# Performance work log

Measured on AMD Instinct MI355X. Metric: run time of the kernel, lower is better.

The kernel has to match this reference:

```python
import jax, jax.numpy as jnp
import numpy as np

P = 16  # patch_size


def _tokenize(x, p):
    # (B,C,H,W) -> (B,C,nP,p,p), row-major patch order
    B, C, H, W = x.shape
    nH, nW = H // p, W // p
    x = x.reshape(B, C, nH, p, nW, p).transpose(0, 1, 2, 4, 3, 5)
    return x.reshape(B, C, nH * nW, p, p)


def _untokenize(t, p, H, W):
    B, C, nP, _, _ = t.shape
    nH, nW = H // p, W // p
    t = t.reshape(B, C, nH, nW, p, p).transpose(0, 1, 2, 4, 3, 5)
    return t.reshape(B, C, H, W)


def _sinusoidal_pe(n, d):
    pos = jnp.arange(n, dtype=jnp.float32)[:, None]                    # (n,1)
    div = jnp.exp(jnp.arange(0, d, 2, dtype=jnp.float32) * (-jnp.log(10000.0) / d))
    ang = pos * div                                                     # (n, d/2)
    pe = jnp.zeros((n, d), dtype=jnp.float32)
    pe = pe.at[:, 0::2].set(jnp.sin(ang))
    pe = pe.at[:, 1::2].set(jnp.cos(ang)[:, : d // 2])
    return pe


def setup_inputs() -> dict:
    key = jax.random.key(0)
    ks = jax.random.split(key, 7)
    B, C, H, W = 16, 3, 512, 512
    nh = 12
    D = C * P * P            # 768 token dim
    dh = D // nh             # 64 head dim
    s = 0.02
    x = jax.random.normal(ks[0], (B, C, H, W), dtype=jnp.float32)
    Wq = jax.random.normal(ks[1], (nh, D, dh), dtype=jnp.float32) * s
    Wk = jax.random.normal(ks[2], (nh, D, dh), dtype=jnp.float32) * s
    Wv = jax.random.normal(ks[3], (nh, D, dh), dtype=jnp.float32) * s
    bq = jax.random.normal(ks[4], (nh, dh), dtype=jnp.float32) * s
    bk = jax.random.normal(ks[5], (nh, dh), dtype=jnp.float32) * s
    bv = jax.random.normal(ks[6], (nh, dh), dtype=jnp.float32) * s
    return {"x": x, "Wq": Wq, "bq": bq, "Wk": Wk, "bk": bk, "Wv": Wv, "bv": bv}


def reference(x, Wq, bq, Wk, bk, Wv, bv):
    B, C, H, W = x.shape
    nh, D, dh = Wq.shape
    tok = _tokenize(x, P)                      # (B,C,nP,p,p)
    nP = tok.shape[2]
    t = tok.reshape(B, nP, D)                  # torch .view semantics (row-major reshape)
    pe = _sinusoidal_pe(nP, D)
    t = 2.0 * t + pe[None]
    # batched per-head projections (H heads, independent weights)
    q = jnp.einsum('bnd,hde->bhne', t, Wq) + bq[None, :, None, :]
    k = jnp.einsum('bnd,hde->bhne', t, Wk) + bk[None, :, None, :]
    v = jnp.einsum('bnd,hde->bhne', t, Wv) + bv[None, :, None, :]
    scores = jnp.einsum('bhne,bhme->bhnm', q, k) / jnp.sqrt(jnp.float32(dh))
    attn = jax.nn.softmax(scores, axis=-1)
    o = jnp.einsum('bhnm,bhme->bhne', attn, v)  # (B,nh,nP,dh)
    # concat heads along last dim
    out = o.transpose(0, 2, 1, 3).reshape(B, nP, D)
    out = out.reshape(B, C, nP, P, P)          # torch .view back
    return _untokenize(out, P, H, W)
```

## Files before the change

kernel.cpp:

```cpp
#include <hip/hip_runtime.h>
#include <hip/hip_bf16.h>
#include <math.h>

typedef short bf16x8 __attribute__((ext_vector_type(8)));
typedef float f32x4 __attribute__((ext_vector_type(4)));

static __device__ __forceinline__ unsigned short f2bf(float f) {
  unsigned int u = __float_as_uint(f);
  u += 0x7FFFu + ((u >> 16) & 1u);
  return (unsigned short)(u >> 16);
}

__global__ __launch_bounds__(256) void k_prep_w(const float* __restrict__ Wq,
                                                const float* __restrict__ Wk,
                                                const float* __restrict__ Wv,
                                                unsigned short* __restrict__ wt) {
  __shared__ unsigned short lw[64][72];
  int sh = blockIdx.x;
  int kt = blockIdx.y;
  int s = sh / 12, h = sh - s * 12;
  const float* W = (s == 0 ? Wq : (s == 1 ? Wk : Wv)) + h * 49152 + (kt << 6) * 64;
  int tid = threadIdx.x;
#pragma unroll
  for (int it = 0; it < 4; ++it) {
    int idx = it * 256 + tid;
    int kk = idx >> 4, e4 = (idx & 15) << 2;
    float4 v = *(const float4*)(W + kk * 64 + e4);
    lw[e4 + 0][kk] = f2bf(v.x);
    lw[e4 + 1][kk] = f2bf(v.y);
    lw[e4 + 2][kk] = f2bf(v.z);
    lw[e4 + 3][kk] = f2bf(v.w);
  }
  __syncthreads();
  unsigned short* outp = wt + sh * 49152 + (kt << 6);
#pragma unroll
  for (int it = 0; it < 2; ++it) {
    int c = it * 256 + tid;
    int e = c >> 3, kc = (c & 7) << 3;
    *(uint4*)(outp + e * 768 + kc) = *(const uint4*)&lw[e][kc];
  }
}

__global__ __launch_bounds__(256) void k_build_t(const float* __restrict__ x,
                                                 unsigned short* __restrict__ t) {
  int g = blockIdx.x * 256 + threadIdx.x;
  int f = g << 3;
  int m  = f / 768;
  int d  = f - m * 768;
  int c  = f >> 18;
  int rl = f & 262143;
  int n  = rl >> 8;
  int qq = rl & 255;
  int ii = qq >> 4, jj = qq & 15;
  float pe8[8];
#pragma unroll
  for (int u = 0; u < 8; ++u) {
    int dd = d + u;
    int k = dd >> 1;
    float ang = (float)m * expf(-0.023985261385f * (float)k);
    pe8[u] = (dd & 1) ? cosf(ang) : sinf(ang);
  }
  const float* xp0 = x + (c << 18) + (((n >> 5) << 4) + ii) * 512 + ((n & 31) << 4) + jj;
  for (int b = 0; b < 16; ++b) {
    const float* xp = xp0 + b * 786432;
    float4 v0 = *(const float4*)xp;
    float4 v1 = *(const float4*)(xp + 4);
    float xv[8] = {v0.x, v0.y, v0.z, v0.w, v1.x, v1.y, v1.z, v1.w};
    unsigned short tmp[8];
#pragma unroll
    for (int u = 0; u < 8; ++u) tmp[u] = f2bf(2.0f * xv[u] + pe8[u]);
    *(uint4*)(t + b * 786432 + f) = *(const uint4*)tmp;
  }
}

union SMQKV {
  struct { unsigned short tA[128][40]; unsigned short tB[64][40]; } g;
  unsigned short tr[64][136];
};
__global__ __launch_bounds__(256) void k_qkv(
    const unsigned short* __restrict__ t, const unsigned short* __restrict__ wt,
    const float* __restrict__ bq, const float* __restrict__ bk, const float* __restrict__ bv,
    unsigned short* __restrict__ qout, unsigned short* __restrict__ kout,
    unsigned short* __restrict__ vout) {
  __shared__ SMQKV sm;
  int bid = blockIdx.x;
  int xcd = bid & 7, idx = bid >> 3;
  int rt = xcd * 16 + idx / 36;
  int hs = idx % 36;
  int h = hs / 3, s = hs - h * 3;
  const unsigned short* Wp = wt + (s * 12 + h) * 49152;
  const float* bias = (s == 0 ? bq : (s == 1 ? bk : bv)) + h * 64;
  unsigned short* outp = (s == 0 ? qout : (s == 1 ? kout : vout));
  int tid = threadIdx.x, lane = tid & 63, w = tid >> 6;
  int row0 = rt << 7;
  f32x4 acc[2][4] = {};
  for (int k0 = 0; k0 < 768; k0 += 32) {
    __syncthreads();
#pragma unroll
    for (int it = 0; it < 2; ++it) {
      int idx2 = it * 256 + tid;
      int rr = idx2 >> 2, kq = (idx2 & 3) << 3;
      *(uint4*)&sm.g.tA[rr][kq] = *(const uint4*)(t + (row0 + rr) * 768 + k0 + kq);
    }
    {
      int e = tid >> 2, kc = (tid & 3) << 3;
      *(uint4*)&sm.g.tB[e][kc] = *(const uint4*)(Wp + e * 768 + k0 + kc);
    }
    __syncthreads();
    bf16x8 a0 = *(const bf16x8*)&sm.g.tA[w * 32 + (lane & 15)][(lane >> 4) << 3];
    bf16x8 a1 = *(const bf16x8*)&sm.g.tA[w * 32 + 16 + (lane & 15)][(lane >> 4) << 3];
#pragma unroll
    for (int cb = 0; cb < 4; ++cb) {
      bf16x8 bb = *(const bf16x8*)&sm.g.tB[cb * 16 + (lane & 15)][(lane >> 4) << 3];
      acc[0][cb] = __builtin_amdgcn_mfma_f32_16x16x32_bf16(a0, bb, acc[0][cb], 0, 0, 0);
      acc[1][cb] = __builtin_amdgcn_mfma_f32_16x16x32_bf16(a1, bb, acc[1][cb], 0, 0, 0);
    }
  }
  int bb2 = row0 >> 10;
  int n0 = row0 & 1023;
  int base = (bb2 * 12 + h) << 16;
  if (s < 2) {
    float qs = (s == 0) ? 0.18033688011f : 1.0f;
#pragma unroll
    for (int mt = 0; mt < 2; ++mt)
#pragma unroll
      for (int cb = 0; cb < 4; ++cb) {
        int e = cb * 16 + (lane & 15);
        float be = bias[e];
#pragma unroll
        for (int r = 0; r < 4; ++r) {
          int n = n0 + w * 32 + mt * 16 + ((lane >> 4) << 2) + r;
          outp[base + (n << 6) + e] = f2bf((acc[mt][cb][r] + be) * qs);
        }
      }
  } else {
    __syncthreads();
#pragma unroll
    for (int mt = 0; mt < 2; ++mt)
#pragma unroll
      for (int cb = 0; cb < 4; ++cb) {
        int e = cb * 16 + (lane & 15);
        float be = bias[e];
#pragma unroll
        for (int r = 0; r < 4; ++r) {
          int rr = w * 32 + ((lane >> 4) << 3) + mt * 4 + r;
          sm.tr[e][rr] = f2bf(acc[mt][cb][r] + be);
        }
      }
    __syncthreads();
#pragma unroll
    for (int it = 0; it < 4; ++it) {
      int c = it * 256 + tid;
      int e = c >> 4, nc = (c & 15) << 3;
      *(uint4*)(vout + base + (e << 10) + n0 + nc) = *(const uint4*)&sm.tr[e][nc];
    }
  }
}

__global__ __launch_bounds__(256) void k_attn(
    const unsigned short* __restrict__ Q,
    const unsigned short* __restrict__ K,
    const unsigned short* __restrict__ Vg,
    float* __restrict__ out) {
  __shared__ unsigned short Kt[64][72];
  __shared__ unsigned short Vt[80][72];
  int bid = blockIdx.x;
  int xcd = bid & 7, idx = bid >> 3;
  int bh = xcd * 24 + (idx >> 3);
  int qt = idx & 7;
  int b = bh / 12, h = bh - b * 12;
  int tid = threadIdx.x, lane = tid & 63, w = tid >> 6;
  int g = lane >> 4, q16 = lane & 15;
  int base = bh << 16;
  const unsigned short* Qp = Q + base + (qt << 7) * 64;
  const unsigned short* Kp = K + base;
  const unsigned short* Vp = Vg + base;
  {
    int rr = 64 + (tid >> 4), c4 = (tid & 15) << 2;
    ushort4 z = {0, 0, 0, 0};
    if ((tid >> 4) == 0) { z.x = z.y = z.z = z.w = 0x3F80; }
    *(ushort4*)&Vt[rr][c4] = z;
  }
  bf16x8 qa[2][2];
#pragma unroll
  for (int mt = 0; mt < 2; ++mt)
#pragma unroll
    for (int kf = 0; kf < 2; ++kf)
      qa[mt][kf] = *(const bf16x8*)(Qp + (w * 32 + mt * 16 + q16) * 64 + kf * 32 + (g << 3));
  f32x4 o[2][5] = {};
  float mrow[2] = {-1e30f, -1e30f};
  for (int kv0 = 0; kv0 < 1024; kv0 += 64) {
    __syncthreads();
#pragma unroll
    for (int it = 0; it < 2; ++it) {
      int idx2 = it * 256 + tid;
      int rr = idx2 >> 3, cc = (idx2 & 7) << 3;
      *(uint4*)&Kt[rr][cc] = *(const uint4*)(Kp + (kv0 << 6) + (idx2 << 3));
      *(uint4*)&Vt[rr][cc] = *(const uint4*)(Vp + (rr << 10) + kv0 + cc);
    }
    __syncthreads();
    f32x4 s[2][4] = {};
#pragma unroll
    for (int cb = 0; cb < 4; ++cb) {
      bf16x8 ka0 = *(const bf16x8*)&Kt[cb * 16 + q16][g << 3];
      bf16x8 ka1 = *(const bf16x8*)&Kt[cb * 16 + q16][32 + (g << 3)];
#pragma unroll
      for (int mt = 0; mt < 2; ++mt) {
        s[mt][cb] = __builtin_amdgcn_mfma_f32_16x16x32_bf16(ka0, qa[mt][0], s[mt][cb], 0, 0, 0);
        s[mt][cb] = __builtin_amdgcn_mfma_f32_16x16x32_bf16(ka1, qa[mt][1], s[mt][cb], 0, 0, 0);
      }
    }
    float pmax[2];
#pragma unroll
    for (int mt = 0; mt < 2; ++mt) {
      float mx = s[mt][0][0];
#pragma unroll
      for (int cb = 0; cb < 4; ++cb)
#pragma unroll
        for (int r = 0; r < 4; ++r) mx = fmaxf(mx, s[mt][cb][r]);
      mx = fmaxf(mx, __shfl_xor(mx, 16));
      mx = fmaxf(mx, __shfl_xor(mx, 32));
      pmax[mt] = mx;
    }
    if (__any((pmax[0] > mrow[0] + 8.f) || (pmax[1] > mrow[1] + 8.f))) {
#pragma unroll
      for (int mt = 0; mt < 2; ++mt) {
        float mnew = fmaxf(mrow[mt], pmax[mt]);
        float sc = __builtin_amdgcn_exp2f(mrow[mt] - mnew);
        mrow[mt] = mnew;
#pragma unroll
        for (int r = 0; r < 4; ++r) {
          float scr = __shfl(sc, (g << 2) + r);
#pragma unroll
          for (int cb = 0; cb < 5; ++cb) o[mt][cb][r] *= scr;
        }
      }
    }
    unsigned int pk[2][4][2];
#pragma unroll
    for (int mt = 0; mt < 2; ++mt)
#pragma unroll
      for (int cb = 0; cb < 4; ++cb)
#pragma unroll
        for (int j2 = 0; j2 < 2; ++j2) {
          float plo = __builtin_amdgcn_exp2f(s[mt][cb][2 * j2] - mrow[mt]);
          float phi = __builtin_amdgcn_exp2f(s[mt][cb][2 * j2 + 1] - mrow[mt]);
          asm("v_cvt_pk_bf16_f32 %0, %1, %2" : "=v"(pk[mt][cb][j2]) : "v"(plo), "v"(phi));
        }
#pragma unroll
    for (int kk = 0; kk < 2; ++kk) {
      union { unsigned int u[4]; bf16x8 v; } pa[2];
#pragma unroll
      for (int mt = 0; mt < 2; ++mt) {
        pa[mt].u[0] = pk[mt][2 * kk][0];
        pa[mt].u[1] = pk[mt][2 * kk][1];
        pa[mt].u[2] = pk[mt][2 * kk + 1][0];
        pa[mt].u[3] = pk[mt][2 * kk + 1][1];
      }
#pragma unroll
      for (int cb = 0; cb < 5; ++cb) {
        bf16x8 vb = *(const bf16x8*)&Vt[cb * 16 + q16][kk * 32 + (g << 3)];
#pragma unroll
        for (int mt = 0; mt < 2; ++mt)
          o[mt][cb] = __builtin_amdgcn_mfma_f32_16x16x32_bf16(pa[mt].v, vb, o[mt][cb], 0, 0, 0);
      }
    }
  }
#pragma unroll
  for (int mt = 0; mt < 2; ++mt)
#pragma unroll
    for (int r = 0; r < 4; ++r) {
      float lr = __shfl(o[mt][4][r], lane & 48);
      float inv = 1.0f / lr;
      int m = (qt << 7) + w * 32 + mt * 16 + (g << 2) + r;
#pragma unroll
      for (int cb = 0; cb < 4; ++cb) {
        int d = (h << 6) + cb * 16 + q16;
        int f = m * 768 + d;
        int c = f >> 18, rl = f & 262143, n = rl >> 8, qq = rl & 255;
        out[((b * 3 + c) << 18) + (((n >> 5) << 4) + (qq >> 4)) * 512 + ((n & 31) << 4) + (qq & 15)] =
            o[mt][cb][r] * inv;
      }
    }
}

extern "C" void kernel_launch(void* const* d_in, const int* in_sizes, int n_in,
                              void* d_out, int out_size, void* d_ws, size_t ws_size,
                              hipStream_t stream) {
  const float* x  = (const float*)d_in[0];
  const float* Wq = (const float*)d_in[1];
  const float* bq = (const float*)d_in[2];
  const float* Wk = (const float*)d_in[3];
  const float* bk = (const float*)d_in[4];
  const float* Wv = (const float*)d_in[5];
  const float* bv = (const float*)d_in[6];
  float* out = (float*)d_out;
  unsigned short* wt = (unsigned short*)d_ws;
  unsigned short* t  = wt + 1769472;
  unsigned short* qw = t  + 12582912;
  unsigned short* kw = qw + 12582912;
  unsigned short* vw = kw + 12582912;
  k_prep_w<<<dim3(36, 12), 256, 0, stream>>>(Wq, Wk, Wv, wt);
  k_build_t<<<384, 256, 0, stream>>>(x, t);
  k_qkv<<<4608, 256, 0, stream>>>(t, wt, bq, bk, bv, qw, kw, vw);
  k_attn<<<1536, 256, 0, stream>>>(qw, kw, vw, out);
}
```

Before: 225.1 us.

## Enlarge QKV GEMM tile to 128x192 with K-step 64

Each block of the QKV projection kernel now computes a 128-row by 192-column tile (three heads of one projection) instead of 128x64. The K step grows from 32 to 64, so activation tiles are reused across more output columns and there are fewer barriers per FLOP. The grid shrinks from 4608 to 1536 blocks, and launch bounds request 3 waves per SIMD. In exchange the kernel needs more LDS and accumulator registers (24 f32x4), which could limit occupancy. The V transpose epilogue now loops over the three heads and packs pairs of bf16 values into 32-bit writes.

```diff
diff --git a/kernel.cpp b/kernel.cpp
--- a/kernel.cpp
+++ b/kernel.cpp
@@ -73,86 +73,100 @@
   }
 }
 
-union SMQKV {
-  struct { unsigned short tA[128][40]; unsigned short tB[64][40]; } g;
-  unsigned short tr[64][136];
+union SMQ {
+  struct { unsigned short A[128][68]; unsigned short Bt[192][68]; } g;
+  unsigned short tr[64][140];
 };
-__global__ __launch_bounds__(256) void k_qkv(
+__global__ __launch_bounds__(256, 3) void k_qkv(
     const unsigned short* __restrict__ t, const unsigned short* __restrict__ wt,
     const float* __restrict__ bq, const float* __restrict__ bk, const float* __restrict__ bv,
     unsigned short* __restrict__ qout, unsigned short* __restrict__ kout,
     unsigned short* __restrict__ vout) {
-  __shared__ SMQKV sm;
+  __shared__ SMQ sm;
   int bid = blockIdx.x;
   int xcd = bid & 7, idx = bid >> 3;
-  int rt = xcd * 16 + idx / 36;
-  int hs = idx % 36;
-  int h = hs / 3, s = hs - h * 3;
-  const unsigned short* Wp = wt + (s * 12 + h) * 49152;
-  const float* bias = (s == 0 ? bq : (s == 1 ? bk : bv)) + h * 64;
+  int rt = xcd * 16 + idx / 12;
+  int ct = idx % 12;
+  int s = ct >> 2;
+  int hbase = (ct & 3) * 3;
+  int row0 = rt << 7;
+  int j0 = ct * 192;
+  const float* bias = (s == 0 ? bq : (s == 1 ? bk : bv));
   unsigned short* outp = (s == 0 ? qout : (s == 1 ? kout : vout));
   int tid = threadIdx.x, lane = tid & 63, w = tid >> 6;
-  int row0 = rt << 7;
-  f32x4 acc[2][4] = {};
-  for (int k0 = 0; k0 < 768; k0 += 32) {
+  int g = lane >> 4, q16 = lane & 15;
+  f32x4 acc[2][12] = {};
+  for (int k0 = 0; k0 < 768; k0 += 64) {
     __syncthreads();
 #pragma unroll
-    for (int it = 0; it < 2; ++it) {
-      int idx2 = it * 256 + tid;
-      int rr = idx2 >> 2, kq = (idx2 & 3) << 3;
-      *(uint4*)&sm.g.tA[rr][kq] = *(const uint4*)(t + (row0 + rr) * 768 + k0 + kq);
-    }
-    {
-      int e = tid >> 2, kc = (tid & 3) << 3;
-      *(uint4*)&sm.g.tB[e][kc] = *(const uint4*)(Wp + e * 768 + k0 + kc);
+    for (int it = 0; it < 4; ++it) {
+      int i2 = it * 256 + tid;
+      int rr = i2 >> 3, ch = (i2 & 7) << 3;
+      *(uint4*)&sm.g.A[rr][ch] = *(const uint4*)(t + (row0 + rr) * 768 + k0 + ch);
+    }
+#pragma unroll
+    for (int it = 0; it < 6; ++it) {
+      int i2 = it * 256 + tid;
+      int rr = i2 >> 3, ch = (i2 & 7) << 3;
+      *(uint4*)&sm.g.Bt[rr][ch] = *(const uint4*)(wt + (j0 + rr) * 768 + k0 + ch);
     }
     __syncthreads();
-    bf16x8 a0 = *(const bf16x8*)&sm.g.tA[w * 32 + (lane & 15)][(lane >> 4) << 3];
-    bf16x8 a1 = *(const bf16x8*)&sm.g.tA[w * 32 + 16 + (lane & 15)][(lane >> 4) << 3];
-#pragma unroll
-    for (int cb = 0; cb < 4; ++cb) {
-      bf16x8 bb = *(const bf16x8*)&sm.g.tB[cb * 16 + (lane & 15)][(lane >> 4) << 3];
-      acc[0][cb] = __builtin_amdgcn_mfma_f32_16x16x32_bf16(a0, bb, acc[0][cb], 0, 0, 0);
-      acc[1][cb] = __builtin_amdgcn_mfma_f32_16x16x32_bf16(a1, bb, acc[1][cb], 0, 0, 0);
-    }
-  }
-  int bb2 = row0 >> 10;
-  int n0 = row0 & 1023;
-  int base = (bb2 * 12 + h) << 16;
+#pragma unroll
+    for (int kk = 0; kk < 2; ++kk) {
+      bf16x8 a0 = *(const bf16x8*)&sm.g.A[w * 32 + q16][kk * 32 + (g << 3)];
+      bf16x8 a1 = *(const bf16x8*)&sm.g.A[w * 32 + 16 + q16][kk * 32 + (g << 3)];
+#pragma unroll
+      for (int cb = 0; cb < 12; ++cb) {
+        bf16x8 bb = *(const bf16x8*)&sm.g.Bt[cb * 16 + q16][kk * 32 + (g << 3)];
+        acc[0][cb] = __builtin_amdgcn_mfma_f32_16x16x32_bf16(a0, bb, acc[0][cb], 0, 0, 0);
+        acc[1][cb] = __builtin_amdgcn_mfma_f32_16x16x32_bf16(a1, bb, acc[1][cb], 0, 0, 0);
+      }
+    }
+  }
+  int bb2 = row0 >> 10, n0 = row0 & 1023;
   if (s < 2) {
     float qs = (s == 0) ? 0.18033688011f : 1.0f;
 #pragma unroll
-    for (int mt = 0; mt < 2; ++mt)
-#pragma unroll
-      for (int cb = 0; cb < 4; ++cb) {
-        int e = cb * 16 + (lane & 15);
-        float be = bias[e];
+    for (int cb = 0; cb < 12; ++cb) {
+      int h = hbase + (cb >> 2);
+      int e = ((cb & 3) << 4) + q16;
+      float be = bias[h * 64 + e];
+      int base = (bb2 * 12 + h) << 16;
+#pragma unroll
+      for (int mt = 0; mt < 2; ++mt)
 #pragma unroll
         for (int r = 0; r < 4; ++r) {
-          int n = n0 + w * 32 + mt * 16 + ((lane >> 4) << 2) + r;
+          int n = n0 + w * 32 + mt * 16 + (g << 2) + r;
           outp[base + (n << 6) + e] = f2bf((acc[mt][cb][r] + be) * qs);
         }
-      }
+    }
   } else {
-    __syncthreads();
-#pragma unroll
-    for (int mt = 0; mt < 2; ++mt)
-#pragma unroll
-      for (int cb = 0; cb < 4; ++cb) {
-        int e = cb * 16 + (lane & 15);
-        float be = bias[e];
-#pragma unroll
-        for (int r = 0; r < 4; ++r) {
-          int rr = w * 32 + ((lane >> 4) << 3) + mt * 4 + r;
-          sm.tr[e][rr] = f2bf(acc[mt][cb][r] + be);
-        }
-      }
-    __syncthreads();
-#pragma unroll
-    for (int it = 0; it < 4; ++it) {
-      int c = it * 256 + tid;
-      int e = c >> 4, nc = (c & 15) << 3;
-      *(uint4*)(vout + base + (e << 10) + n0 + nc) = *(const uint4*)&sm.tr[e][nc];
+#pragma unroll
+    for (int hc = 0; hc < 3; ++hc) {
+      __syncthreads();
+#pragma unroll
+      for (int cq = 0; cq < 4; ++cq) {
+        int cb = hc * 4 + cq;
+        int e = (cq << 4) + q16;
+        float be = bias[(hbase + hc) * 64 + e];
+#pragma unroll
+        for (int mt = 0; mt < 2; ++mt)
+#pragma unroll
+          for (int rp = 0; rp < 2; ++rp) {
+            int rr = w * 32 + (g << 3) + mt * 4 + rp * 2;
+            unsigned int lo = f2bf(acc[mt][cb][rp * 2] + be);
+            unsigned int hi = f2bf(acc[mt][cb][rp * 2 + 1] + be);
+            *(unsigned int*)&sm.tr[e][rr] = lo | (hi << 16);
+          }
+      }
+      __syncthreads();
+      int base = ((bb2 * 12 + hbase + hc) << 16);
+#pragma unroll
+      for (int it = 0; it < 4; ++it) {
+        int c = it * 256 + tid;
+        int e = c >> 4, nc = (c & 15) << 3;
+        *(uint4*)(vout + base + (e << 10) + n0 + nc) = *(const uint4*)&sm.tr[e][nc];
+      }
     }
   }
 }
@@ -302,6 +316,6 @@
   unsigned short* vw = kw + 12582912;
   k_prep_w<<<dim3(36, 12), 256, 0, stream>>>(Wq, Wk, Wv, wt);
   k_build_t<<<384, 256, 0, stream>>>(x, t);
-  k_qkv<<<4608, 256, 0, stream>>>(t, wt, bq, bk, bv, qw, kw, vw);
+  k_qkv<<<1536, 256, 0, stream>>>(t, wt, bq, bk, bv, qw, kw, vw);
   k_attn<<<1536, 256, 0, stream>>>(qw, kw, vw, out);
 }
```

New measurement: 367.9 us. +63.4%, slower.
